# Kernel tuning notes

Hardware: AMD Instinct MI355X
Metric: run time of the kernel (lower is better)

Reference implementation:

```python
import jax, jax.numpy as jnp
import numpy as np

VOXEL_SCALE = 20.0   # cfg.SPARSE3D.VOXEL_SCALE (metric -> voxel pixels)
POOLER_SCALE = 0.25  # cfg.MODEL.ROI_BOX_HEAD.POOLER_SCALES_SPATIAL[0]
RES = 7              # pooler resolution per axis
EPS = 1e-5           # BatchNorm eps


def _roi_align_3d(feat, boxes_px, batch_idx, res):
    """3D ROIAlign, sampling_ratio=1 (one trilinear sample per bin).
    feat: [B, X, Y, Z, C] channels-last; boxes_px: [N,6] = (x1,y1,z1,x2,y2,z2)
    in feature-map coordinates. Returns [N, C, res, res, res]."""
    B, X, Y, Z, C = feat.shape
    N = boxes_px.shape[0]
    start, end = boxes_px[:, :3], boxes_px[:, 3:]
    size = jnp.maximum(end - start, 1.0)            # [N,3] legacy min roi size
    binsz = size / res
    off = jnp.arange(res, dtype=boxes_px.dtype) + 0.5
    px = start[:, 0:1] + off[None, :] * binsz[:, 0:1]   # [N,res]
    py = start[:, 1:2] + off[None, :] * binsz[:, 1:2]
    pz = start[:, 2:3] + off[None, :] * binsz[:, 2:3]
    P = res * res * res
    PX = jnp.broadcast_to(px[:, :, None, None], (N, res, res, res)).reshape(N, P)
    PY = jnp.broadcast_to(py[:, None, :, None], (N, res, res, res)).reshape(N, P)
    PZ = jnp.broadcast_to(pz[:, None, None, :], (N, res, res, res)).reshape(N, P)

    def corners(p, dim):
        p0 = jnp.floor(p)
        frac = p - p0
        i0 = jnp.clip(p0.astype(jnp.int32), 0, dim - 1)
        i1 = jnp.clip(p0.astype(jnp.int32) + 1, 0, dim - 1)
        return i0, i1, frac

    x0, x1, lx = corners(PX, X)
    y0, y1, ly = corners(PY, Y)
    z0, z1, lz = corners(PZ, Z)
    feat_flat = feat.reshape(B * X * Y * Z, C)
    base = batch_idx.astype(jnp.int32)[:, None]          # [N,1]
    acc = jnp.zeros((N, P, C), feat.dtype)
    for dx in (0, 1):  # 8 trilinear corners; fixed small loop
        xi, wx = (x0, 1.0 - lx) if dx == 0 else (x1, lx)
        for dy in (0, 1):
            yi, wy = (y0, 1.0 - ly) if dy == 0 else (y1, ly)
            for dz in (0, 1):
                zi, wz = (z0, 1.0 - lz) if dz == 0 else (z1, lz)
                lin = ((base * X + xi) * Y + yi) * Z + zi  # [N,P]
                acc = acc + (wx * wy * wz)[:, :, None] * feat_flat[lin]
    pooled = acc.reshape(N, res, res, res, C)  # 1 sample per bin -> no avg
    return pooled.transpose(0, 4, 1, 2, 3)     # [N, C, rx, ry, rz]


def setup_inputs():
    key = jax.random.key(0)
    ks = jax.random.split(key, 8)
    B, C, X, Y, Z = 2, 128, 80, 80, 20
    N, rep = 1024, 128 * RES              # rep = OUT_CHANNELS * pooler_z = 896
    in_size = C * RES * RES * RES         # 43904
    features = jax.random.normal(ks[0], (B, X, Y, Z, C), jnp.float32)
    ext = jnp.array([16.0, 16.0, 4.0], jnp.float32)  # metric extent = dim/(voxel_scale*pooler_scale)
    ctr = jax.random.uniform(ks[1], (N, 3), jnp.float32) * ext
    half = 0.25 + jax.random.uniform(ks[2], (N, 3), jnp.float32) * 1.75
    boxes = jnp.concatenate([ctr - half, ctr + half], axis=1)  # metric units
    batch_idx = jax.random.randint(ks[3], (N,), 0, B, jnp.int32)
    conv_w = jax.random.normal(ks[4], (rep, C, RES), jnp.float32) * 0.02
    conv_b = jnp.zeros((rep,), jnp.float32)
    gamma = jnp.ones((rep,), jnp.float32)
    beta = jnp.zeros((rep,), jnp.float32)
    fc6_w = jax.random.normal(ks[5], (in_size, rep), jnp.float32) * np.float32(1.0 / np.sqrt(in_size))
    fc6_b = jnp.zeros((rep,), jnp.float32)
    fc7_w = jax.random.normal(ks[6], (rep, rep), jnp.float32) * np.float32(1.0 / np.sqrt(rep))
    fc7_b = jnp.zeros((rep,), jnp.float32)
    return dict(features=features, boxes=boxes, conv_w=conv_w, conv_b=conv_b,
                gamma=gamma, beta=beta, fc6_w=fc6_w, fc6_b=fc6_b,
                fc7_w=fc7_w, fc7_b=fc7_b, batch_idx=batch_idx)


def reference(features, boxes, conv_w, conv_b, gamma, beta,
              fc6_w, fc6_b, fc7_w, fc7_b, batch_idx):
    # convert_metric_to_pixel (x voxel_scale) fused with pooler spatial scale
    boxes_px = boxes * (VOXEL_SCALE * POOLER_SCALE)
    pooled = _roi_align_3d(features, boxes_px, batch_idx, RES)  # [N,C,7,7,7]
    # conv3d kernel [1,1,Z]: contract channels and z -> [N, rep, 7, 7]
    y = jnp.einsum('ncxyz,rcz->nrxy', pooled, conv_w) + conv_b[None, :, None, None]
    # BatchNorm3d, training-mode batch statistics per channel
    mu = y.mean(axis=(0, 2, 3), keepdims=True)
    var = ((y - mu) ** 2).mean(axis=(0, 2, 3), keepdims=True)
    y = (y - mu) * jax.lax.rsqrt(var + EPS) * gamma[None, :, None, None] + beta[None, :, None, None]
    y = jax.nn.relu(y)
    x2 = y.reshape(y.shape[0], -1)                   # [N, rep*49] == [N, C*343]
    x3 = jax.nn.relu(x2 @ fc6_w + fc6_b)
    x4 = jax.nn.relu(x3 @ fc7_w + fc7_b)
    return x4
```

## Files before the change

kernel.cpp:

```cpp
#include <hip/hip_runtime.h>
#include <cstdint>

typedef unsigned short u16;
using bf16x8  = __attribute__((ext_vector_type(8))) __bf16;
using floatx4 = __attribute__((ext_vector_type(4))) float;

__device__ __forceinline__ u16 f2bf(float f) {
    uint32_t u = __builtin_bit_cast(uint32_t, f);
    u += 0x7fffu + ((u >> 16) & 1u);
    return (u16)(u >> 16);
}
__device__ __forceinline__ float bf2f(u16 h) {
    uint32_t u = ((uint32_t)h) << 16;
    return __builtin_bit_cast(float, u);
}

__global__ __launch_bounds__(256) void k_roialign(
    const float* __restrict__ feat, const float* __restrict__ boxes,
    const int* __restrict__ bidx, u16* __restrict__ A1)
{
    const int n = blockIdx.x;
    const int t = threadIdx.x;
    const float s = 5.0f;
    const float x1 = boxes[n*6+0]*s, y1 = boxes[n*6+1]*s, z1 = boxes[n*6+2]*s;
    const float x2 = boxes[n*6+3]*s, y2 = boxes[n*6+4]*s, z2 = boxes[n*6+5]*s;
    const float binx = fmaxf(x2-x1, 1.0f) * (1.0f/7.0f);
    const float biny = fmaxf(y2-y1, 1.0f) * (1.0f/7.0f);
    const float binz = fmaxf(z2-z1, 1.0f) * (1.0f/7.0f);
    const int b = bidx[n];
    const float* fb = feat + (size_t)b * 80 * 80 * 20 * 128;
    const int c4   = (t & 31) * 4;
    const int slot = t >> 5;

    for (int p = slot; p < 343; p += 8) {
        const int xq = p / 49;
        const int rem = p - xq * 49;
        const int yq = rem / 7;
        const int zq = rem - yq * 7;
        const float px = x1 + ((float)xq + 0.5f) * binx;
        const float py = y1 + ((float)yq + 0.5f) * biny;
        const float pz = z1 + ((float)zq + 0.5f) * binz;
        const float fx = floorf(px), fy = floorf(py), fz = floorf(pz);
        const float lx = px - fx, ly = py - fy, lz = pz - fz;
        const int xi0 = min(max((int)fx,     0), 79);
        const int xi1 = min(max((int)fx + 1, 0), 79);
        const int yi0 = min(max((int)fy,     0), 79);
        const int yi1 = min(max((int)fy + 1, 0), 79);
        const int zi0 = min(max((int)fz,     0), 19);
        const int zi1 = min(max((int)fz + 1, 0), 19);
        const float wx0 = 1.f-lx, wy0 = 1.f-ly, wz0 = 1.f-lz;
        const float w00 = wx0*wy0, w01 = wx0*ly, w10 = lx*wy0, w11 = lx*ly;
        float a0=0.f, a1=0.f, a2=0.f, a3=0.f;
#define RC(W, XI, YI, ZI) { \
        const float4 v = *(const float4*)(fb + (size_t)(((XI)*80+(YI))*20+(ZI))*128 + c4); \
        a0 = fmaf((W), v.x, a0); a1 = fmaf((W), v.y, a1); \
        a2 = fmaf((W), v.z, a2); a3 = fmaf((W), v.w, a3); }
        RC(w00*wz0, xi0, yi0, zi0); RC(w00*lz, xi0, yi0, zi1);
        RC(w01*wz0, xi0, yi1, zi0); RC(w01*lz, xi0, yi1, zi1);
        RC(w10*wz0, xi1, yi0, zi0); RC(w10*lz, xi1, yi0, zi1);
        RC(w11*wz0, xi1, yi1, zi0); RC(w11*lz, xi1, yi1, zi1);
#undef RC
        const int m = n * 49 + xq * 7 + yq;
        ushort4 o;
        o.x = f2bf(a0); o.y = f2bf(a1); o.z = f2bf(a2); o.w = f2bf(a3);
        *(ushort4*)(A1 + (size_t)m * 896 + zq * 128 + c4) = o;
    }
}

__global__ __launch_bounds__(256) void k_prep_wc(
    const float* __restrict__ w, u16* __restrict__ out)
{
    const int i = blockIdx.x * 256 + threadIdx.x;
    const int r = i / 896, k = i % 896;
    const int z = k >> 7, c = k & 127;
    out[i] = f2bf(w[(r * 128 + c) * 7 + z]);
}

template <int PERM>
__global__ __launch_bounds__(256) void k_transpose(
    const float* __restrict__ in, u16* __restrict__ out, int Kin)
{
    __shared__ u16 tile[64][72];
    const int kp0 = blockIdx.x * 64, r0 = blockIdx.y * 64;
    const int t = threadIdx.x;
#pragma unroll
    for (int it = 0; it < 16; ++it) {
        const int idx = it * 256 + t;
        const int i = idx >> 6, rl = idx & 63;
        const int kp = kp0 + i;
        const int k = PERM ? (kp % 896) * 49 + (kp / 896) : kp;
        tile[i][rl] = f2bf(in[(size_t)k * 896 + r0 + rl]);
    }
    __syncthreads();
#pragma unroll
    for (int it = 0; it < 16; ++it) {
        const int idx = it * 256 + t;
        const int rl = idx >> 6, i = idx & 63;
        out[(size_t)(r0 + rl) * Kin + kp0 + i] = tile[i][rl];
    }
}

template <int EPI>
__global__ __launch_bounds__(256) void k_gemm(
    const u16* __restrict__ A, const u16* __restrict__ Bt,
    float* __restrict__ outF, u16* __restrict__ outH,
    const float* __restrict__ bias, float* __restrict__ bnsum, float* __restrict__ bnsq,
    int Astride, int Bstride, int kpc, int ktot, int partStride)
{
    __shared__ __align__(16) u16 lA[128 * 40];
    __shared__ __align__(16) u16 lB[128 * 40];
    const int t = threadIdx.x;
    const int wave = t >> 6, lane = t & 63;
    const int wm = wave & 1, wn = wave >> 1;
    const int quad = lane >> 4, lr = lane & 15;
    const size_t m0 = (size_t)blockIdx.x * 128;
    const size_t n0 = (size_t)blockIdx.y * 128;
    const int kbeg = blockIdx.z * kpc;
    const int kend = min(kbeg + kpc, ktot);

    floatx4 acc[4][4];
    const floatx4 zero = {0.f, 0.f, 0.f, 0.f};
#pragma unroll
    for (int a = 0; a < 4; ++a)
#pragma unroll
        for (int bq = 0; bq < 4; ++bq) acc[a][bq] = zero;

    const int e0 = t * 8;
    const int r0s = e0 >> 5, c0s = e0 & 31;
    const int e1 = e0 + 2048;
    const int r1s = e1 >> 5, c1s = e1 & 31;
    const u16* Ab = A + m0 * (size_t)Astride;
    const u16* Bb = Bt + n0 * (size_t)Bstride;

    for (int ks = kbeg; ks < kend; ++ks) {
        const size_t k0 = (size_t)ks * 32;
        const uint4 va0 = *(const uint4*)(Ab + (size_t)r0s * Astride + k0 + c0s);
        const uint4 va1 = *(const uint4*)(Ab + (size_t)r1s * Astride + k0 + c1s);
        const uint4 vb0 = *(const uint4*)(Bb + (size_t)r0s * Bstride + k0 + c0s);
        const uint4 vb1 = *(const uint4*)(Bb + (size_t)r1s * Bstride + k0 + c1s);
        __syncthreads();
        *(uint4*)(lA + r0s * 40 + c0s) = va0;
        *(uint4*)(lA + r1s * 40 + c1s) = va1;
        *(uint4*)(lB + r0s * 40 + c0s) = vb0;
        *(uint4*)(lB + r1s * 40 + c1s) = vb1;
        __syncthreads();
        bf16x8 af[4], bfr[4];
#pragma unroll
        for (int mt = 0; mt < 4; ++mt)
            af[mt] = *(const bf16x8*)(lA + (wm * 64 + mt * 16 + lr) * 40 + quad * 8);
#pragma unroll
        for (int nt = 0; nt < 4; ++nt)
            bfr[nt] = *(const bf16x8*)(lB + (wn * 64 + nt * 16 + lr) * 40 + quad * 8);
#pragma unroll
        for (int mt = 0; mt < 4; ++mt)
#pragma unroll
            for (int nt = 0; nt < 4; ++nt)
                acc[mt][nt] = __builtin_amdgcn_mfma_f32_16x16x32_bf16(
                    af[mt], bfr[nt], acc[mt][nt], 0, 0, 0);
    }

    if (EPI == 0) {
#pragma unroll
        for (int nt = 0; nt < 4; ++nt) {
            const int n = (int)n0 + wn * 64 + nt * 16 + lr;
            const float bv = bias[n];
            float s1 = 0.f, s2 = 0.f;
#pragma unroll
            for (int mt = 0; mt < 4; ++mt) {
#pragma unroll
                for (int j = 0; j < 4; ++j) {
                    const int m = (int)m0 + wm * 64 + mt * 16 + quad * 4 + j;
                    const float v = acc[mt][nt][j] + bv;
                    outH[(size_t)m * 896 + n] = f2bf(v);
                    s1 += v;
                    s2 = fmaf(v, v, s2);
                }
            }
            s1 += __shfl_xor(s1, 16); s1 += __shfl_xor(s1, 32);
            s2 += __shfl_xor(s2, 16); s2 += __shfl_xor(s2, 32);
            if (quad == 0) {
                atomicAdd(&bnsum[n], s1);
                atomicAdd(&bnsq[n],  s2);
            }
        }
    } else {
        float* po = outF + (size_t)blockIdx.z * partStride;
#pragma unroll
        for (int nt = 0; nt < 4; ++nt) {
            const int n = (int)n0 + wn * 64 + nt * 16 + lr;
#pragma unroll
            for (int mt = 0; mt < 4; ++mt) {
#pragma unroll
                for (int j = 0; j < 4; ++j) {
                    const int m = (int)m0 + wm * 64 + mt * 16 + quad * 4 + j;
                    po[(size_t)m * 896 + n] = acc[mt][nt][j];
                }
            }
        }
    }
}

__global__ __launch_bounds__(256) void k_bn_apply(
    u16* __restrict__ y, const float* __restrict__ s1, const float* __restrict__ s2,
    const float* __restrict__ gamma, const float* __restrict__ beta)
{
    const size_t i = ((size_t)blockIdx.x * 256 + threadIdx.x) * 8;
    uint4 d = *(const uint4*)(y + i);
    const u16* h = (const u16*)&d;
    const int r0 = (int)(i % 896);
    __align__(16) u16 o[8];
    const float invM = 1.0f / 50176.0f;
#pragma unroll
    for (int j = 0; j < 8; ++j) {
        const int r = r0 + j;
        const float mu  = s1[r] * invM;
        const float var = fmaf(-mu, mu, s2[r] * invM);
        const float rs  = rsqrtf(var + 1e-5f);
        const float v   = (bf2f(h[j]) - mu) * rs * gamma[r] + beta[r];
        o[j] = f2bf(fmaxf(v, 0.f));
    }
    *(uint4*)(y + i) = *(const uint4*)o;
}

__global__ __launch_bounds__(256) void k_x3(
    const float* __restrict__ part, const float* __restrict__ bias, u16* __restrict__ x3)
{
    const size_t i = ((size_t)blockIdx.x * 256 + threadIdx.x) * 4;
    float a0=0.f, a1=0.f, a2=0.f, a3=0.f;
#pragma unroll
    for (int c = 0; c < 16; ++c) {
        const float4 v = *(const float4*)(part + (size_t)c * 917504 + i);
        a0 += v.x; a1 += v.y; a2 += v.z; a3 += v.w;
    }
    const int r = (int)(i % 896);
    ushort4 o;
    o.x = f2bf(fmaxf(a0 + bias[r+0], 0.f));
    o.y = f2bf(fmaxf(a1 + bias[r+1], 0.f));
    o.z = f2bf(fmaxf(a2 + bias[r+2], 0.f));
    o.w = f2bf(fmaxf(a3 + bias[r+3], 0.f));
    *(ushort4*)(x3 + i) = o;
}

__global__ __launch_bounds__(256) void k_out(
    const float* __restrict__ part, const float* __restrict__ bias, float* __restrict__ out)
{
    const size_t i = ((size_t)blockIdx.x * 256 + threadIdx.x) * 4;
    float a0=0.f, a1=0.f, a2=0.f, a3=0.f;
#pragma unroll
    for (int c = 0; c < 4; ++c) {
        const float4 v = *(const float4*)(part + (size_t)c * 917504 + i);
        a0 += v.x; a1 += v.y; a2 += v.z; a3 += v.w;
    }
    const int r = (int)(i % 896);
    float4 o;
    o.x = fmaxf(a0 + bias[r+0], 0.f);
    o.y = fmaxf(a1 + bias[r+1], 0.f);
    o.z = fmaxf(a2 + bias[r+2], 0.f);
    o.w = fmaxf(a3 + bias[r+3], 0.f);
    *(float4*)(out + i) = o;
}

extern "C" void kernel_launch(void* const* d_in, const int* in_sizes, int n_in,
                              void* d_out, int out_size, void* d_ws, size_t ws_size,
                              hipStream_t stream)
{
    (void)in_sizes; (void)n_in; (void)out_size; (void)ws_size;
    const float* features = (const float*)d_in[0];
    const float* boxes    = (const float*)d_in[1];
    const float* conv_w   = (const float*)d_in[2];
    const float* conv_b   = (const float*)d_in[3];
    const float* gamma    = (const float*)d_in[4];
    const float* beta     = (const float*)d_in[5];
    const float* fc6_w    = (const float*)d_in[6];
    const float* fc6_b    = (const float*)d_in[7];
    const float* fc7_w    = (const float*)d_in[8];
    const float* fc7_b    = (const float*)d_in[9];
    const int*   batch_idx = (const int*)d_in[10];
    float* out = (float*)d_out;
    char* ws = (char*)d_ws;

    size_t off = 0;
    auto alloc = [&](size_t b) { size_t o = off; off += (b + 255) & ~(size_t)255; return o; };
    const size_t oA1   = alloc(50176ull * 896 * 2);
    const size_t oWcT  = alloc(896ull * 896 * 2);
    const size_t oY    = alloc(50176ull * 896 * 2);
    const size_t oF6T  = alloc(43904ull * 896 * 2);
    const size_t oF7T  = alloc(896ull * 896 * 2);
    const size_t oStat = alloc(8192);
    const size_t oP2 = oA1;
    const size_t oX3 = oA1 + 58720256;
    const size_t oP3 = oX3 + 1835008;

    u16*   A1    = (u16*)(ws + oA1);
    u16*   WcT   = (u16*)(ws + oWcT);
    u16*   Y     = (u16*)(ws + oY);
    u16*   F6T   = (u16*)(ws + oF6T);
    u16*   F7T   = (u16*)(ws + oF7T);
    float* bnsum = (float*)(ws + oStat);
    float* bnsq  = bnsum + 1024;
    float* P2    = (float*)(ws + oP2);
    u16*   X3    = (u16*)(ws + oX3);
    float* P3    = (float*)(ws + oP3);

    k_prep_wc<<<3136, 256, 0, stream>>>(conv_w, WcT);
    k_transpose<1><<<dim3(686, 14), 256, 0, stream>>>(fc6_w, F6T, 43904);
    k_transpose<0><<<dim3(14, 14), 256, 0, stream>>>(fc7_w, F7T, 896);
    hipMemsetAsync(ws + oStat, 0, 8192, stream);

    k_roialign<<<1024, 256, 0, stream>>>(features, boxes, batch_idx, A1);

    k_gemm<0><<<dim3(392, 7, 1), 256, 0, stream>>>(
        A1, WcT, nullptr, Y, conv_b, bnsum, bnsq, 896, 896, 28, 28, 0);

    k_bn_apply<<<21952, 256, 0, stream>>>(Y, bnsum, bnsq, gamma, beta);

    k_gemm<1><<<dim3(8, 7, 16), 256, 0, stream>>>(
        Y, F6T, P2, nullptr, nullptr, nullptr, nullptr, 43904, 43904, 86, 1372, 917504);
    k_x3<<<896, 256, 0, stream>>>(P2, fc6_b, X3);

    k_gemm<1><<<dim3(8, 7, 4), 256, 0, stream>>>(
        X3, F7T, P3, nullptr, nullptr, nullptr, nullptr, 896, 896, 7, 28, 917504);
    k_out<<<896, 256, 0, stream>>>(P3, fc7_b, out);
}
```

Before: 813.4 us.

## Load GEMM tiles directly into LDS and swizzle conv-GEMM block order

```diff
diff --git a/kernel.cpp b/kernel.cpp
--- a/kernel.cpp
+++ b/kernel.cpp
@@ -13,6 +13,13 @@
 __device__ __forceinline__ float bf2f(u16 h) {
     uint32_t u = ((uint32_t)h) << 16;
     return __builtin_bit_cast(float, u);
+}
+
+__device__ __forceinline__ void gload16(const u16* g, u16* l) {
+    __builtin_amdgcn_global_load_lds(
+        (const __attribute__((address_space(1))) unsigned int*)g,
+        (__attribute__((address_space(3))) unsigned int*)l,
+        16, 0, 0);
 }
 
 __global__ __launch_bounds__(256) void k_roialign(
@@ -107,15 +114,24 @@
     const float* __restrict__ bias, float* __restrict__ bnsum, float* __restrict__ bnsq,
     int Astride, int Bstride, int kpc, int ktot, int partStride)
 {
-    __shared__ __align__(16) u16 lA[128 * 40];
-    __shared__ __align__(16) u16 lB[128 * 40];
+    __shared__ __align__(16) u16 lA[128 * 32];
+    __shared__ __align__(16) u16 lB[128 * 32];
     const int t = threadIdx.x;
     const int wave = t >> 6, lane = t & 63;
     const int wm = wave & 1, wn = wave >> 1;
     const int quad = lane >> 4, lr = lane & 15;
-    const size_t m0 = (size_t)blockIdx.x * 128;
-    const size_t n0 = (size_t)blockIdx.y * 128;
-    const int kbeg = blockIdx.z * kpc;
+
+    int mt, nt, kz;
+    if (EPI == 0) {
+        const int wg = blockIdx.x;
+        const int swz = (wg & 7) * 343 + (wg >> 3);
+        nt = swz % 7; mt = swz / 7; kz = 0;
+    } else {
+        mt = blockIdx.x; nt = blockIdx.y; kz = blockIdx.z;
+    }
+    const size_t m0 = (size_t)mt * 128;
+    const size_t n0 = (size_t)nt * 128;
+    const int kbeg = kz * kpc;
     const int kend = min(kbeg + kpc, ktot);
 
     floatx4 acc[4][4];
@@ -125,52 +141,52 @@
 #pragma unroll
         for (int bq = 0; bq < 4; ++bq) acc[a][bq] = zero;
 
-    const int e0 = t * 8;
-    const int r0s = e0 >> 5, c0s = e0 & 31;
-    const int e1 = e0 + 2048;
-    const int r1s = e1 >> 5, c1s = e1 & 31;
-    const u16* Ab = A + m0 * (size_t)Astride;
-    const u16* Bb = Bt + n0 * (size_t)Bstride;
+    const int ch0 = wave * 2, ch1 = ch0 + 1;
+    const int sr0 = ch0 * 16 + (lane >> 2);
+    const int sr1 = sr0 + 16;
+    const int sc  = (lane & 3) * 8;
+    const u16* gA0 = A  + (m0 + sr0) * (size_t)Astride + (size_t)kbeg * 32 + sc;
+    const u16* gA1 = A  + (m0 + sr1) * (size_t)Astride + (size_t)kbeg * 32 + sc;
+    const u16* gB0 = Bt + (n0 + sr0) * (size_t)Bstride + (size_t)kbeg * 32 + sc;
+    const u16* gB1 = Bt + (n0 + sr1) * (size_t)Bstride + (size_t)kbeg * 32 + sc;
+    u16* lA0 = lA + ch0 * 512;
+    u16* lA1 = lA + ch1 * 512;
+    u16* lB0 = lB + ch0 * 512;
+    u16* lB1 = lB + ch1 * 512;
 
     for (int ks = kbeg; ks < kend; ++ks) {
-        const size_t k0 = (size_t)ks * 32;
-        const uint4 va0 = *(const uint4*)(Ab + (size_t)r0s * Astride + k0 + c0s);
-        const uint4 va1 = *(const uint4*)(Ab + (size_t)r1s * Astride + k0 + c1s);
-        const uint4 vb0 = *(const uint4*)(Bb + (size_t)r0s * Bstride + k0 + c0s);
-        const uint4 vb1 = *(const uint4*)(Bb + (size_t)r1s * Bstride + k0 + c1s);
         __syncthreads();
-        *(uint4*)(lA + r0s * 40 + c0s) = va0;
-        *(uint4*)(lA + r1s * 40 + c1s) = va1;
-        *(uint4*)(lB + r0s * 40 + c0s) = vb0;
-        *(uint4*)(lB + r1s * 40 + c1s) = vb1;
+        gload16(gA0, lA0); gload16(gA1, lA1);
+        gload16(gB0, lB0); gload16(gB1, lB1);
+        gA0 += 32; gA1 += 32; gB0 += 32; gB1 += 32;
         __syncthreads();
         bf16x8 af[4], bfr[4];
 #pragma unroll
-        for (int mt = 0; mt < 4; ++mt)
-            af[mt] = *(const bf16x8*)(lA + (wm * 64 + mt * 16 + lr) * 40 + quad * 8);
-#pragma unroll
-        for (int nt = 0; nt < 4; ++nt)
-            bfr[nt] = *(const bf16x8*)(lB + (wn * 64 + nt * 16 + lr) * 40 + quad * 8);
-#pragma unroll
-        for (int mt = 0; mt < 4; ++mt)
-#pragma unroll
-            for (int nt = 0; nt < 4; ++nt)
-                acc[mt][nt] = __builtin_amdgcn_mfma_f32_16x16x32_bf16(
-                    af[mt], bfr[nt], acc[mt][nt], 0, 0, 0);
+        for (int mt4 = 0; mt4 < 4; ++mt4)
+            af[mt4] = *(const bf16x8*)(lA + (wm * 64 + mt4 * 16 + lr) * 32 + quad * 8);
+#pragma unroll
+        for (int nt4 = 0; nt4 < 4; ++nt4)
+            bfr[nt4] = *(const bf16x8*)(lB + (wn * 64 + nt4 * 16 + lr) * 32 + quad * 8);
+#pragma unroll
+        for (int mt4 = 0; mt4 < 4; ++mt4)
+#pragma unroll
+            for (int nt4 = 0; nt4 < 4; ++nt4)
+                acc[mt4][nt4] = __builtin_amdgcn_mfma_f32_16x16x32_bf16(
+                    af[mt4], bfr[nt4], acc[mt4][nt4], 0, 0, 0);
     }
 
     if (EPI == 0) {
 #pragma unroll
-        for (int nt = 0; nt < 4; ++nt) {
-            const int n = (int)n0 + wn * 64 + nt * 16 + lr;
+        for (int nt4 = 0; nt4 < 4; ++nt4) {
+            const int n = (int)n0 + wn * 64 + nt4 * 16 + lr;
             const float bv = bias[n];
             float s1 = 0.f, s2 = 0.f;
 #pragma unroll
-            for (int mt = 0; mt < 4; ++mt) {
+            for (int mt4 = 0; mt4 < 4; ++mt4) {
 #pragma unroll
                 for (int j = 0; j < 4; ++j) {
-                    const int m = (int)m0 + wm * 64 + mt * 16 + quad * 4 + j;
-                    const float v = acc[mt][nt][j] + bv;
+                    const int m = (int)m0 + wm * 64 + mt4 * 16 + quad * 4 + j;
+                    const float v = acc[mt4][nt4][j] + bv;
                     outH[(size_t)m * 896 + n] = f2bf(v);
                     s1 += v;
                     s2 = fmaf(v, v, s2);
@@ -186,14 +202,14 @@
     } else {
         float* po = outF + (size_t)blockIdx.z * partStride;
 #pragma unroll
-        for (int nt = 0; nt < 4; ++nt) {
-            const int n = (int)n0 + wn * 64 + nt * 16 + lr;
-#pragma unroll
-            for (int mt = 0; mt < 4; ++mt) {
+        for (int nt4 = 0; nt4 < 4; ++nt4) {
+            const int n = (int)n0 + wn * 64 + nt4 * 16 + lr;
+#pragma unroll
+            for (int mt4 = 0; mt4 < 4; ++mt4) {
 #pragma unroll
                 for (int j = 0; j < 4; ++j) {
-                    const int m = (int)m0 + wm * 64 + mt * 16 + quad * 4 + j;
-                    po[(size_t)m * 896 + n] = acc[mt][nt][j];
+                    const int m = (int)m0 + wm * 64 + mt4 * 16 + quad * 4 + j;
+                    po[(size_t)m * 896 + n] = acc[mt4][nt4][j];
                 }
             }
         }
@@ -309,7 +325,7 @@
 
     k_roialign<<<1024, 256, 0, stream>>>(features, boxes, batch_idx, A1);
 
-    k_gemm<0><<<dim3(392, 7, 1), 256, 0, stream>>>(
+    k_gemm<0><<<dim3(2744, 1, 1), 256, 0, stream>>>(
         A1, WcT, nullptr, Y, conv_b, bnsum, bnsq, 896, 896, 28, 28, 0);
 
     k_bn_apply<<<21952, 256, 0, stream>>>(Y, bnsum, bnsq, gamma, beta);
```

Measured after the change: 770.1 us. 5.3% less time.
